# Kernel tuning notes

Hardware: AMD Instinct MI355X
Metric: run time of the kernel (lower is better)

Reference implementation:

```python
import jax, jax.numpy as jnp
import numpy as np

N = 10000
E = 160000
F_IN = 64
HID = 128
HEADS = 8
NC = 3
NEG_SLOPE = 0.2
EPS = 1e-16


def setup_inputs() -> dict:
    key = jax.random.key(0)
    ks = jax.random.split(key, 12)
    p = lambda k, shape: jax.random.normal(k, shape, jnp.float32) * 0.1
    return {
        "x": jax.random.normal(ks[0], (N, F_IN), jnp.float32),
        "edge_index": jax.random.randint(ks[1], (2, E), 0, N),
        # conv1: F_IN -> 8 heads x 128, concat -> 1024
        "W1": p(ks[2], (F_IN, HEADS * HID)),
        "a_src1": p(ks[3], (HEADS, HID)),
        "a_dst1": p(ks[4], (HEADS, HID)),
        "b1": jnp.zeros((HEADS * HID,), jnp.float32),
        # conv2: 1024 -> 8 heads x 64, concat -> 512
        "W2": p(ks[5], (HEADS * HID, HEADS * (HID // 2))),
        "a_src2": p(ks[6], (HEADS, HID // 2)),
        "a_dst2": p(ks[7], (HEADS, HID // 2)),
        "b2": jnp.zeros((HEADS * (HID // 2),), jnp.float32),
        # conv3: 512 -> 1 head x 3, mean (concat=False)
        "W3": p(ks[8], (HEADS * (HID // 2), NC)),
        "a_src3": p(ks[9], (1, NC)),
        "a_dst3": p(ks[10], (1, NC)),
        "b3": jnp.zeros((NC,), jnp.float32),
    }


def gat_conv(x, src, dst, W, a_src, a_dst, b, concat):
    """PyG-style GATConv (eval mode, self-loops already in src/dst)."""
    n = x.shape[0]
    H, C = a_src.shape
    h = (x @ W).reshape(n, H, C)                      # [N, H, C]
    s_src = jnp.sum(h * a_src[None], axis=-1)         # [N, H]
    s_dst = jnp.sum(h * a_dst[None], axis=-1)         # [N, H]
    e = jax.nn.leaky_relu(s_src[src] + s_dst[dst], NEG_SLOPE)  # [E, H]
    # segment softmax over incoming edges per destination node
    m = jax.ops.segment_max(e, dst, num_segments=n)   # [N, H]
    ex = jnp.exp(e - m[dst])
    denom = jax.ops.segment_sum(ex, dst, num_segments=n)
    alpha = ex / (denom[dst] + EPS)                   # [E, H]
    msg = h[src] * alpha[:, :, None]                  # [E, H, C]
    out = jax.ops.segment_sum(msg, dst, num_segments=n)  # [N, H, C]
    out = out.reshape(n, H * C) if concat else out.mean(axis=1)
    return out + b


def reference(x, edge_index, W1, a_src1, a_dst1, b1, W2, a_src2, a_dst2, b2, W3, a_src3, a_dst3, b3):
    n = x.shape[0]
    loop = jnp.arange(n, dtype=edge_index.dtype)
    src = jnp.concatenate([edge_index[0], loop])
    dst = jnp.concatenate([edge_index[1], loop])
    h = gat_conv(x, src, dst, W1, a_src1, a_dst1, b1, True)
    h = jax.nn.elu(h)
    h = gat_conv(h, src, dst, W2, a_src2, a_dst2, b2, True)
    h = jax.nn.elu(h)
    h = gat_conv(h, src, dst, W3, a_src3, a_dst3, b3, False)
    return jax.nn.log_softmax(h, axis=1)
```

## Files before the change

### kernel.cpp

```cpp
#include <hip/hip_runtime.h>
#include <math.h>

#define NEG_SLOPE 0.2f
#define EPS_DEN 1e-16f

typedef __attribute__((ext_vector_type(8))) short bf16x8;
typedef __attribute__((ext_vector_type(4))) float f32x4;

__device__ inline unsigned short f2bf(float f) {
    unsigned u = __float_as_uint(f);
    return (unsigned short)((u + 0x7FFFu + ((u >> 16) & 1u)) >> 16);
}
__device__ inline float bflo(unsigned u) { return __uint_as_float(u << 16); }
__device__ inline float bfhi(unsigned u) { return __uint_as_float(u & 0xFFFF0000u); }

__global__ __launch_bounds__(256) void k_pre(const int* __restrict__ ei, int E, int Nn,
                                             int* __restrict__ counts,
                                             const float* __restrict__ x, short* __restrict__ A1, int Mp,
                                             const float* __restrict__ W1, short* __restrict__ B1t,
                                             const float* __restrict__ W2, short* __restrict__ B2t) {
    __shared__ float s[32][33];
    int t = threadIdx.x;
    int b = blockIdx.x;
    int ET = E + Nn;
    int etb = (ET + 255) / 256;
    int xb = (Mp * 64 + 255) / 256;
    if (b < etb) {
        int e = b * 256 + t;
        if (e < ET) {
            int d = (e < E) ? ei[E + e] : (e - E);
            atomicAdd(&counts[d], 1);
        }
        return;
    }
    b -= etb;
    if (b < xb) {
        int i = b * 256 + t;
        if (i < Mp * 64) {
            int row = i >> 6, c = i & 63;
            float v = (row < Nn) ? x[(size_t)row * 64 + c] : 0.f;
            A1[(size_t)row * 64 + c] = (short)f2bf(v);
        }
        return;
    }
    b -= xb;
    const float* W; short* Bt; int K, N, kb, nb;
    if (b < 64) {
        W = W1; Bt = B1t; K = 64; N = 1024;
        kb = b & 1; nb = b >> 1;
    } else {
        b -= 64;
        W = W2; Bt = B2t; K = 1024; N = 512;
        kb = b & 31; nb = b >> 5;
    }
    int k0 = kb * 32, n0 = nb * 32;
    int tx = t & 31, ty = t >> 5;
    for (int r = ty; r < 32; r += 8) s[r][tx] = W[(size_t)(k0 + r) * N + n0 + tx];
    __syncthreads();
    for (int r = ty; r < 32; r += 8) {
        float v = s[tx][r];
        Bt[(size_t)(n0 + r) * K + k0 + tx] = (short)f2bf(v);
    }
}

__global__ void k_scan(const int* __restrict__ counts, int Nn, int ET, int* __restrict__ row_off) {
    __shared__ int lds[256];
    int t = threadIdx.x;
    int chunk = (Nn + 255) / 256;
    int b0 = t * chunk, b1 = min(Nn, b0 + chunk);
    int s = 0;
    for (int i = b0; i < b1; i++) s += counts[i];
    lds[t] = s;
    __syncthreads();
    #pragma unroll
    for (int d = 1; d < 256; d <<= 1) {
        int v = (t >= d) ? lds[t - d] : 0;
        __syncthreads();
        lds[t] += v;
        __syncthreads();
    }
    int run = (t == 0) ? 0 : lds[t - 1];
    for (int i = b0; i < b1; i++) { row_off[i] = run; run += counts[i]; }
    if (t == 0) row_off[Nn] = ET;
}

__global__ void k_scatter(const int* __restrict__ ei, int E, int Nn,
                          const int* __restrict__ row_off, int* cursor, int* __restrict__ col) {
    int e = blockIdx.x * blockDim.x + threadIdx.x;
    int ET = E + Nn;
    if (e >= ET) return;
    int d = (e < E) ? ei[E + e] : (e - E);
    int s = (e < E) ? ei[e] : (e - E);
    int pos = atomicAdd(&cursor[d], 1);
    col[row_off[d] + pos] = s;
}

template<int HEADC>
__global__ __launch_bounds__(256) void k_mfma_w(const short* __restrict__ A,
                                                const short* __restrict__ B,
                                                unsigned short* __restrict__ C,
                                                const float* __restrict__ a_src,
                                                const float* __restrict__ a_dst,
                                                float* __restrict__ ssrc,
                                                float* __restrict__ sdst,
                                                int M, int N, int Ktot,
                                                int lda, int ldb) {
    __shared__ short As[64 * 32];
    __shared__ short Bs[128 * 32];
    __shared__ float sred[4][64][2];
    int t = threadIdx.x;
    int lane = t & 63;
    int wid = t >> 6;

    int nbx = N >> 7;
    int nb = gridDim.x;
    int q = nb >> 3, r = nb & 7;
    int xcd = blockIdx.x & 7, pos = blockIdx.x >> 3;
    int L = (xcd < r ? xcd * (q + 1) : r * (q + 1) + (xcd - r) * q) + pos;
    int bn = (L % nbx) * 128;
    int bm = (L / nbx) * 64;

    int wm = (wid & 1) * 32, wn = (wid >> 1) * 64;
    int fr = lane & 15, kq = lane >> 4;

    int srow = t >> 2, sslot = t & 3;
    int sko = ((sslot ^ ((srow >> 1) & 3)) << 3);

    f32x4 acc[2][4] = {};

    for (int k0 = 0; k0 < Ktot; k0 += 32) {
        {
            const short* sa = A + (size_t)(bm + srow) * lda + k0 + sko;
            short* da = As + (size_t)(wid << 6) * 8;
            __builtin_amdgcn_global_load_lds((const __attribute__((address_space(1))) void*)sa,
                                             (__attribute__((address_space(3))) void*)da, 16, 0, 0);
            #pragma unroll
            for (int qq = 0; qq < 2; qq++) {
                int v = qq * 256 + t;
                int rowb = v >> 2, slotb = v & 3;
                int skob = ((slotb ^ ((rowb >> 1) & 3)) << 3);
                const short* sb = B + (size_t)(bn + rowb) * ldb + k0 + skob;
                short* db = Bs + (size_t)(qq * 256 + (wid << 6)) * 8;
                __builtin_amdgcn_global_load_lds((const __attribute__((address_space(1))) void*)sb,
                                                 (__attribute__((address_space(3))) void*)db, 16, 0, 0);
            }
        }
        __syncthreads();
        bf16x8 af[2], bfv[4];
        #pragma unroll
        for (int i = 0; i < 2; i++) {
            int rowa = wm + i * 16 + fr;
            af[i] = *(const bf16x8*)(As + rowa * 32 + ((kq ^ ((rowa >> 1) & 3)) << 3));
        }
        #pragma unroll
        for (int j = 0; j < 4; j++) {
            int rowb = wn + j * 16 + fr;
            bfv[j] = *(const bf16x8*)(Bs + rowb * 32 + ((kq ^ ((rowb >> 1) & 3)) << 3));
        }
        #pragma unroll
        for (int i = 0; i < 2; i++)
            #pragma unroll
            for (int j = 0; j < 4; j++)
                acc[i][j] = __builtin_amdgcn_mfma_f32_16x16x32_bf16(af[i], bfv[j], acc[i][j], 0, 0, 0);
        __syncthreads();
    }
    #pragma unroll
    for (int i = 0; i < 2; i++) {
        int rbase = bm + wm + i * 16 + kq * 4;
        #pragma unroll
        for (int j = 0; j < 4; j++) {
            int colc = bn + wn + j * 16 + fr;
            #pragma unroll
            for (int rg = 0; rg < 4; rg++) {
                int rr = rbase + rg;
                if (rr < M) C[(size_t)rr * N + colc] = f2bf(acc[i][j][rg]);
            }
        }
    }
    float asv[4], adv[4];
    #pragma unroll
    for (int j = 0; j < 4; j++) {
        int colc = bn + wn + j * 16 + fr;
        asv[j] = a_src[colc];
        adv[j] = a_dst[colc];
    }
    float ps[8], pd[8];
    #pragma unroll
    for (int i = 0; i < 2; i++)
        #pragma unroll
        for (int rg = 0; rg < 4; rg++) {
            int k8 = i * 4 + rg;
            ps[k8] = acc[i][0][rg] * asv[0] + acc[i][1][rg] * asv[1]
                   + acc[i][2][rg] * asv[2] + acc[i][3][rg] * asv[3];
            pd[k8] = acc[i][0][rg] * adv[0] + acc[i][1][rg] * adv[1]
                   + acc[i][2][rg] * adv[2] + acc[i][3][rg] * adv[3];
        }
    #pragma unroll
    for (int k8 = 0; k8 < 8; k8++) {
        #pragma unroll
        for (int off = 1; off < 16; off <<= 1) {
            ps[k8] += __shfl_xor(ps[k8], off);
            pd[k8] += __shfl_xor(pd[k8], off);
        }
    }
    if (HEADC == 128) {
        if (fr == 0) {
            #pragma unroll
            for (int i = 0; i < 2; i++)
                #pragma unroll
                for (int rg = 0; rg < 4; rg++) {
                    int rl = wm + i * 16 + kq * 4 + rg;
                    sred[wid][rl][0] = ps[i * 4 + rg];
                    sred[wid][rl][1] = pd[i * 4 + rg];
                }
        }
        __syncthreads();
        if (wid < 2 && fr == 0) {
            int hh = bn >> 7;
            #pragma unroll
            for (int i = 0; i < 2; i++)
                #pragma unroll
                for (int rg = 0; rg < 4; rg++) {
                    int rl = wm + i * 16 + kq * 4 + rg;
                    int rr = bm + rl;
                    if (rr < M) {
                        ssrc[rr * 8 + hh] = sred[wid][rl][0] + sred[wid + 2][rl][0];
                        sdst[rr * 8 + hh] = sred[wid][rl][1] + sred[wid + 2][rl][1];
                    }
                }
        }
    } else {
        int hh = (bn + wn) >> 6;
        if (fr == 0) {
            #pragma unroll
            for (int i = 0; i < 2; i++)
                #pragma unroll
                for (int rg = 0; rg < 4; rg++) {
                    int rr = bm + wm + i * 16 + kq * 4 + rg;
                    if (rr < M) {
                        ssrc[rr * 8 + hh] = ps[i * 4 + rg];
                        sdst[rr * 8 + hh] = pd[i * 4 + rg];
                    }
                }
        }
    }
}

template<int H, int C, int CB, bool ELU, bool BFOUT>
__global__ __launch_bounds__(256) void k_agg_wave(const unsigned short* __restrict__ hsrc,
                                                  const float* __restrict__ ssrc,
                                                  const float* __restrict__ sdst,
                                                  const int* __restrict__ col,
                                                  const int* __restrict__ row_off,
                                                  const float* __restrict__ bias,
                                                  float* __restrict__ out,
                                                  unsigned short* __restrict__ osp,
                                                  int nw) {
    constexpr int D = H * C;
    int lane = threadIdx.x & 63;
    int w = blockIdx.x * 4 + (threadIdx.x >> 6);
    if (w >= nw) return;
    int n, cb;
    if (CB == 2) { n = w >> 1; cb = w & 1; } else { n = w; cb = 0; }
    int col0 = cb * 512 + lane * 8;
    int myhead = col0 / C;
    float sd = sdst[n * H + myhead];
    int beg = row_off[n], end = row_off[n + 1];
    const unsigned short* hbase = hsrc + col0;

    float acc[8] = {0.f, 0.f, 0.f, 0.f, 0.f, 0.f, 0.f, 0.f};
    float den = 0.f;
    #pragma unroll 4
    for (int j = beg; j < end; j++) {
        int cj = col[j];
        float s = ssrc[cj * H + myhead] + sd;
        s = (s >= 0.f) ? s : NEG_SLOPE * s;
        float ex = __expf(s);
        den += ex;
        uint4 u = *(const uint4*)(hbase + (size_t)cj * D);
        acc[0] += ex * bflo(u.x); acc[1] += ex * bfhi(u.x);
        acc[2] += ex * bflo(u.y); acc[3] += ex * bfhi(u.y);
        acc[4] += ex * bflo(u.z); acc[5] += ex * bfhi(u.z);
        acc[6] += ex * bflo(u.w); acc[7] += ex * bfhi(u.w);
    }
    float iv = 1.f / (den + EPS_DEN);
    float vals[8];
    #pragma unroll
    for (int v = 0; v < 8; v++) {
        float val = acc[v] * iv + bias[col0 + v];
        if (ELU) val = (val > 0.f) ? val : (__expf(val) - 1.f);
        vals[v] = val;
    }
    if (BFOUT) {
        uint4 o;
        o.x = (unsigned)f2bf(vals[0]) | ((unsigned)f2bf(vals[1]) << 16);
        o.y = (unsigned)f2bf(vals[2]) | ((unsigned)f2bf(vals[3]) << 16);
        o.z = (unsigned)f2bf(vals[4]) | ((unsigned)f2bf(vals[5]) << 16);
        o.w = (unsigned)f2bf(vals[6]) | ((unsigned)f2bf(vals[7]) << 16);
        *(uint4*)(osp + (size_t)n * D + col0) = o;
    } else {
        *(f32x4*)(out + (size_t)n * D + col0) = *(f32x4*)&vals[0];
        *(f32x4*)(out + (size_t)n * D + col0 + 4) = *(f32x4*)&vals[4];
    }
}

__global__ __launch_bounds__(256) void k_agg2_l3(const unsigned short* __restrict__ hsrc,
                                                 const float* __restrict__ ssrc,
                                                 const float* __restrict__ sdst,
                                                 const int* __restrict__ col,
                                                 const int* __restrict__ row_off,
                                                 const float* __restrict__ bias,
                                                 const float* __restrict__ W3,
                                                 const float* __restrict__ as3,
                                                 const float* __restrict__ ad3,
                                                 float4* __restrict__ h3s,
                                                 float* __restrict__ sdst3,
                                                 int Nn) {
    constexpr int D = 512;
    __shared__ float cacc[2][64][9];
    int t = threadIdx.x;
    int lane = t & 63;
    int wid = t >> 6;
    int node_i = wid >> 1, half = wid & 1;
    int n = blockIdx.x * 2 + node_i;
    bool active = (n < Nn);
    int col0 = lane * 8;
    int myhead = lane >> 3;
    float acc[8] = {0.f, 0.f, 0.f, 0.f, 0.f, 0.f, 0.f, 0.f};
    float den = 0.f;
    if (active) {
        float sd = sdst[n * 8 + myhead];
        int beg = row_off[n], end = row_off[n + 1];
        const unsigned short* hbase = hsrc + col0;
        #pragma unroll 4
        for (int j = beg + half; j < end; j += 2) {
            int cj = col[j];
            float s = ssrc[cj * 8 + myhead] + sd;
            s = (s >= 0.f) ? s : NEG_SLOPE * s;
            float ex = __expf(s);
            den += ex;
            uint4 u = *(const uint4*)(hbase + (size_t)cj * D);
            acc[0] += ex * bflo(u.x); acc[1] += ex * bfhi(u.x);
            acc[2] += ex * bflo(u.y); acc[3] += ex * bfhi(u.y);
            acc[4] += ex * bflo(u.z); acc[5] += ex * bfhi(u.z);
            acc[6] += ex * bflo(u.w); acc[7] += ex * bfhi(u.w);
        }
    }
    if (half == 1) {
        #pragma unroll
        for (int v = 0; v < 8; v++) cacc[node_i][lane][v] = acc[v];
        cacc[node_i][lane][8] = den;
    }
    __syncthreads();
    if (half == 0 && active) {
        #pragma unroll
        for (int v = 0; v < 8; v++) acc[v] += cacc[node_i][lane][v];
        den += cacc[node_i][lane][8];
        float iv = 1.f / (den + EPS_DEN);
        float t0 = 0.f, t1 = 0.f, t2 = 0.f;
        #pragma unroll
        for (int v = 0; v < 8; v++) {
            float val = acc[v] * iv + bias[col0 + v];
            val = (val > 0.f) ? val : (__expf(val) - 1.f);
            const float* wp = W3 + (size_t)(col0 + v) * 3;
            t0 += val * wp[0];
            t1 += val * wp[1];
            t2 += val * wp[2];
        }
        #pragma unroll
        for (int off = 32; off >= 1; off >>= 1) {
            t0 += __shfl_xor(t0, off);
            t1 += __shfl_xor(t1, off);
            t2 += __shfl_xor(t2, off);
        }
        if (lane == 0) {
            float s3 = t0 * as3[0] + t1 * as3[1] + t2 * as3[2];
            h3s[n] = make_float4(t0, t1, t2, s3);
            sdst3[n] = t0 * ad3[0] + t1 * ad3[1] + t2 * ad3[2];
        }
    }
}

__global__ __launch_bounds__(256) void k_l3_fused(const float4* __restrict__ h3s,
                                                  const float* __restrict__ sdst, const int* __restrict__ col,
                                                  const int* __restrict__ row_off, const float* __restrict__ b3,
                                                  float* __restrict__ out, int Nn) {
    int n = blockIdx.x * 64 + (threadIdx.x >> 2);
    int l4 = threadIdx.x & 3;
    if (n >= Nn) return;
    int beg = row_off[n], end = row_off[n + 1];
    float sd = sdst[n];
    float den = 0.f, a0 = 0.f, a1 = 0.f, a2 = 0.f;
    for (int j = beg + l4; j < end; j += 4) {
        int sI = col[j];
        float4 v = h3s[sI];
        float s = v.w + sd;
        s = (s >= 0.f) ? s : NEG_SLOPE * s;
        float ex = __expf(s);
        den += ex;
        a0 += ex * v.x;
        a1 += ex * v.y;
        a2 += ex * v.z;
    }
    #pragma unroll
    for (int off = 1; off <= 2; off <<= 1) {
        den += __shfl_xor(den, off);
        a0 += __shfl_xor(a0, off);
        a1 += __shfl_xor(a1, off);
        a2 += __shfl_xor(a2, off);
    }
    if (l4 == 0) {
        float iv = 1.f / (den + EPS_DEN);
        float v0 = a0 * iv + b3[0], v1 = a1 * iv + b3[1], v2 = a2 * iv + b3[2];
        float m = fmaxf(v0, fmaxf(v1, v2));
        float l = logf(__expf(v0 - m) + __expf(v1 - m) + __expf(v2 - m));
        out[n * 3 + 0] = v0 - m - l;
        out[n * 3 + 1] = v1 - m - l;
        out[n * 3 + 2] = v2 - m - l;
    }
}

extern "C" void kernel_launch(void* const* d_in, const int* in_sizes, int n_in,
                              void* d_out, int out_size, void* d_ws, size_t ws_size,
                              hipStream_t stream) {
    (void)n_in; (void)out_size; (void)ws_size;
    const float* x   = (const float*)d_in[0];
    const int*   ei  = (const int*)d_in[1];
    const float* W1  = (const float*)d_in[2];
    const float* as1 = (const float*)d_in[3];
    const float* ad1 = (const float*)d_in[4];
    const float* b1  = (const float*)d_in[5];
    const float* W2  = (const float*)d_in[6];
    const float* as2 = (const float*)d_in[7];
    const float* ad2 = (const float*)d_in[8];
    const float* b2  = (const float*)d_in[9];
    const float* W3  = (const float*)d_in[10];
    const float* as3 = (const float*)d_in[11];
    const float* ad3 = (const float*)d_in[12];
    const float* b3  = (const float*)d_in[13];
    float* out = (float*)d_out;

    const int Nn = in_sizes[0] / 64;
    const int E  = in_sizes[1] / 2;
    const int ET = E + Nn;
    const int Mp = ((Nn + 127) / 128) * 128;

    char* ws = (char*)d_ws;
    size_t off = 0;
    auto alloc = [&](size_t bytes) -> void* {
        void* p = ws + off;
        off = (off + bytes + 255) & ~(size_t)255;
        return p;
    };
    unsigned short* hbuf = (unsigned short*)alloc((size_t)Mp * 1024 * 2);
    unsigned short* A2   = (unsigned short*)alloc((size_t)Mp * 1024 * 2);
    float4* h3s = (float4*)alloc((size_t)Nn * 16);
    short* A1   = (short*)alloc((size_t)Mp * 64 * 2);
    short* B1t  = (short*)alloc((size_t)1024 * 64 * 2);
    short* B2t  = (short*)alloc((size_t)512 * 1024 * 2);
    float* ssrc = (float*)alloc((size_t)Nn * 8 * 4);
    float* sdst = (float*)alloc((size_t)Nn * 8 * 4);
    float* ssrcB= (float*)alloc((size_t)Nn * 8 * 4);
    float* sdstB= (float*)alloc((size_t)Nn * 8 * 4);
    float* sdst3= (float*)alloc((size_t)Nn * 4);
    int* counts = (int*)alloc((size_t)Nn * 2 * 4);
    int* cursor = counts + Nn;
    int* row_off= (int*)alloc((size_t)(Nn + 1) * 4);
    int* colb   = (int*)alloc((size_t)ET * 4);

    hipMemsetAsync(counts, 0, (size_t)Nn * 2 * 4, stream);

    int etb = (ET + 255) / 256;
    int xb = (Mp * 64 + 255) / 256;
    int preb = etb + xb + 64 + 512;
    k_pre<<<preb, 256, 0, stream>>>(ei, E, Nn, counts, x, A1, Mp, W1, B1t, W2, B2t);
    k_scan<<<1, 256, 0, stream>>>(counts, Nn, ET, row_off);
    k_scatter<<<etb, 256, 0, stream>>>(ei, E, Nn, row_off, cursor, colb);

    {
        int nb = (1024 / 128) * (Mp / 64);
        k_mfma_w<128><<<nb, 256, 0, stream>>>(A1, B1t, hbuf, as1, ad1, ssrc, sdst,
                                              Nn, 1024, 64, 64, 64);
        int nw = Nn * 2;
        k_agg_wave<8, 128, 2, true, true><<<(nw + 3) / 4, 256, 0, stream>>>(
            hbuf, ssrc, sdst, colb, row_off, b1, nullptr, A2, nw);
    }
    {
        int nb = (512 / 128) * (Mp / 64);
        k_mfma_w<64><<<nb, 256, 0, stream>>>((const short*)A2, B2t, hbuf, as2, ad2, ssrcB, sdstB,
                                             Nn, 512, 1024, 1024, 1024);
        k_agg2_l3<<<(Nn + 1) / 2, 256, 0, stream>>>(hbuf, ssrcB, sdstB, colb, row_off, b2,
                                                    W3, as3, ad3, h3s, sdst3, Nn);
    }
    k_l3_fused<<<(Nn + 63) / 64, 256, 0, stream>>>(h3s, sdst3, colb, row_off, b3, out, Nn);
}
```

Measured before the change: 167.6 us.

## Split layer-1 aggregation into XCD-aware column slices for L2 locality

Replaces the generic wave-per-half-row aggregation with a dedicated layer-1 kernel. Each wave now handles a quarter of the 1024 feature columns (4 bf16 values per lane), and blocks are mapped so that every column slice always lands on the same pair of XCDs. Each XCD's L2 therefore caches only its slice of the gathered neighbour features, which is meant to raise L2 hit rates for the random source gathers. The cost is twice as many waves, narrower 8-byte loads, and repeated per-edge score and exp computation across the four slices.

```diff
diff --git a/kernel.cpp b/kernel.cpp
--- a/kernel.cpp
+++ b/kernel.cpp
@@ -246,62 +246,51 @@
     }
 }
 
-template<int H, int C, int CB, bool ELU, bool BFOUT>
-__global__ __launch_bounds__(256) void k_agg_wave(const unsigned short* __restrict__ hsrc,
-                                                  const float* __restrict__ ssrc,
-                                                  const float* __restrict__ sdst,
-                                                  const int* __restrict__ col,
-                                                  const int* __restrict__ row_off,
-                                                  const float* __restrict__ bias,
-                                                  float* __restrict__ out,
-                                                  unsigned short* __restrict__ osp,
-                                                  int nw) {
-    constexpr int D = H * C;
+__global__ __launch_bounds__(256) void k_agg1_x(const unsigned short* __restrict__ hsrc,
+                                                const float* __restrict__ ssrc,
+                                                const float* __restrict__ sdst,
+                                                const int* __restrict__ col,
+                                                const int* __restrict__ row_off,
+                                                const float* __restrict__ bias,
+                                                unsigned short* __restrict__ osp,
+                                                int Nn) {
+    constexpr int D = 1024;
     int lane = threadIdx.x & 63;
-    int w = blockIdx.x * 4 + (threadIdx.x >> 6);
-    if (w >= nw) return;
-    int n, cb;
-    if (CB == 2) { n = w >> 1; cb = w & 1; } else { n = w; cb = 0; }
-    int col0 = cb * 512 + lane * 8;
-    int myhead = col0 / C;
-    float sd = sdst[n * H + myhead];
+    int wid = threadIdx.x >> 6;
+    int xcd = blockIdx.x & 7, pos = blockIdx.x >> 3;
+    int slice = xcd & 3;
+    int n = pos * 8 + ((xcd >> 2) << 2) + wid;
+    if (n >= Nn) return;
+    int col0 = slice * 256 + lane * 4;
+    int myhead = col0 >> 7;
+    float sd = sdst[n * 8 + myhead];
     int beg = row_off[n], end = row_off[n + 1];
     const unsigned short* hbase = hsrc + col0;
 
-    float acc[8] = {0.f, 0.f, 0.f, 0.f, 0.f, 0.f, 0.f, 0.f};
+    float acc[4] = {0.f, 0.f, 0.f, 0.f};
     float den = 0.f;
     #pragma unroll 4
     for (int j = beg; j < end; j++) {
         int cj = col[j];
-        float s = ssrc[cj * H + myhead] + sd;
+        float s = ssrc[cj * 8 + myhead] + sd;
         s = (s >= 0.f) ? s : NEG_SLOPE * s;
         float ex = __expf(s);
         den += ex;
-        uint4 u = *(const uint4*)(hbase + (size_t)cj * D);
+        uint2 u = *(const uint2*)(hbase + (size_t)cj * D);
         acc[0] += ex * bflo(u.x); acc[1] += ex * bfhi(u.x);
         acc[2] += ex * bflo(u.y); acc[3] += ex * bfhi(u.y);
-        acc[4] += ex * bflo(u.z); acc[5] += ex * bfhi(u.z);
-        acc[6] += ex * bflo(u.w); acc[7] += ex * bfhi(u.w);
     }
     float iv = 1.f / (den + EPS_DEN);
-    float vals[8];
-    #pragma unroll
-    for (int v = 0; v < 8; v++) {
+    float vals[4];
+    #pragma unroll
+    for (int v = 0; v < 4; v++) {
         float val = acc[v] * iv + bias[col0 + v];
-        if (ELU) val = (val > 0.f) ? val : (__expf(val) - 1.f);
-        vals[v] = val;
-    }
-    if (BFOUT) {
-        uint4 o;
-        o.x = (unsigned)f2bf(vals[0]) | ((unsigned)f2bf(vals[1]) << 16);
-        o.y = (unsigned)f2bf(vals[2]) | ((unsigned)f2bf(vals[3]) << 16);
-        o.z = (unsigned)f2bf(vals[4]) | ((unsigned)f2bf(vals[5]) << 16);
-        o.w = (unsigned)f2bf(vals[6]) | ((unsigned)f2bf(vals[7]) << 16);
-        *(uint4*)(osp + (size_t)n * D + col0) = o;
-    } else {
-        *(f32x4*)(out + (size_t)n * D + col0) = *(f32x4*)&vals[0];
-        *(f32x4*)(out + (size_t)n * D + col0 + 4) = *(f32x4*)&vals[4];
-    }
+        vals[v] = (val > 0.f) ? val : (__expf(val) - 1.f);
+    }
+    uint2 o;
+    o.x = (unsigned)f2bf(vals[0]) | ((unsigned)f2bf(vals[1]) << 16);
+    o.y = (unsigned)f2bf(vals[2]) | ((unsigned)f2bf(vals[3]) << 16);
+    *(uint2*)(osp + (size_t)n * D + col0) = o;
 }
 
 __global__ __launch_bounds__(256) void k_agg2_l3(const unsigned short* __restrict__ hsrc,
@@ -481,9 +470,8 @@
         int nb = (1024 / 128) * (Mp / 64);
         k_mfma_w<128><<<nb, 256, 0, stream>>>(A1, B1t, hbuf, as1, ad1, ssrc, sdst,
                                               Nn, 1024, 64, 64, 64);
-        int nw = Nn * 2;
-        k_agg_wave<8, 128, 2, true, true><<<(nw + 3) / 4, 256, 0, stream>>>(
-            hbuf, ssrc, sdst, colb, row_off, b1, nullptr, A2, nw);
+        int nblk = (Nn + 7) / 8 * 8;
+        k_agg1_x<<<nblk, 256, 0, stream>>>(hbuf, ssrc, sdst, colb, row_off, b1, A2, Nn);
     }
     {
         int nb = (512 / 128) * (Mp / 64);
```

Measured after the change: 162.9 us. 2.8% less time.
